# Performance work log

Hardware: AMD Instinct MI355X
Metric: run time of the kernel (lower is better)

Reference implementation:

```python
import jax, jax.numpy as jnp
import numpy as np

HEAD = 4

def setup_inputs() -> dict:
    key = jax.random.key(0)
    ks = jax.random.split(key, 6)
    b, h, w, dim, attn_dim = 2, 64, 64, 256, 128
    return {
        "query": jax.random.normal(ks[0], (b, h, w, dim), jnp.float32),
        "context": jax.random.normal(ks[1], (b, h, w, dim), jnp.float32),
        "Wq": jax.random.normal(ks[2], (dim, attn_dim), jnp.float32) * (dim ** -0.5),
        "Wk": jax.random.normal(ks[3], (dim, attn_dim), jnp.float32) * (dim ** -0.5),
        "Wv": jax.random.normal(ks[4], (dim, attn_dim), jnp.float32) * (dim ** -0.5),
        "Wo": jax.random.normal(ks[5], (attn_dim, dim), jnp.float32) * (attn_dim ** -0.5),
    }

def reference(query, context, Wq, Wk, Wv, Wo):
    b, h, w, c = query.shape
    attn_dim = Wq.shape[1]
    head = HEAD
    head_dim = attn_dim // head
    scale = head_dim ** -0.5
    n = h * w
    # 1x1 conv, no bias == per-pixel dense projection
    q = (query.reshape(b, n, c) @ Wq).reshape(b, n, head, head_dim)
    k = (context.reshape(b, n, c) @ Wk).reshape(b, n, head, head_dim)
    v = (context.reshape(b, n, c) @ Wv).reshape(b, n, head, head_dim)
    score = jnp.einsum('bihd,bjhd->bijh', q, k) * scale  # [b, n, n, head]
    attn = jax.nn.softmax(score, axis=-2)  # softmax over key axis j
    out = jnp.einsum('bijh,bjhd->bihd', attn, v).reshape(b, n, attn_dim)
    return (out @ Wo).reshape(b, h, w, c)
```

## Files before the change

### kernel.cpp

```cpp
#include <hip/hip_runtime.h>
#include <hip/hip_bf16.h>
#include <math.h>

#define N_TOK 4096
#define C_DIM 256
#define A_DIM 128
#define HEADS 4
#define HD    32
#define NBAT  2
#define BH    (NBAT * HEADS)

#define SCALE_LOG2E 0.25503521f

#define SPLITS 8
#define KEYS_PER_SPLIT (N_TOK / SPLITS)

#define KS 40
#define VS 72
#define PS 40

typedef __attribute__((ext_vector_type(8))) short short8;
typedef __attribute__((ext_vector_type(4))) short short4_t;
typedef __attribute__((ext_vector_type(4))) float floatx4;

__device__ __forceinline__ unsigned short f2bf(float f) {
    unsigned int u = __float_as_uint(f);
    u = (u + 0x7fffu + ((u >> 16) & 1u)) >> 16;
    return (unsigned short)u;
}
__device__ __forceinline__ float bf2f(unsigned short u) {
    return __uint_as_float((unsigned int)u << 16);
}
__device__ __forceinline__ unsigned int pack2(float a, float b) {
    unsigned int lo = (__float_as_uint(a) + 0x8000u) >> 16;
    unsigned int hi = (__float_as_uint(b) + 0x8000u) & 0xffff0000u;
    return hi | lo;
}

__global__ __launch_bounds__(256) void wpack_kernel(
    const float* __restrict__ Wq, const float* __restrict__ Wk,
    const float* __restrict__ Wv, const float* __restrict__ Wo,
    unsigned short* __restrict__ Wp)
{
    const int chunk = blockIdx.x * 256 + threadIdx.x;
    const int wid = chunk >> 12;
    const int c = chunk & 4095;
    const int lane = c & 63, quad = lane >> 4, l15 = lane & 15;
    short8 v;
    if (wid < 3) {
        const int s = c >> 9, t = (c >> 6) & 7;
        const float* W = (wid == 0) ? Wq : ((wid == 1) ? Wk : Wv);
        const float scale = (wid == 0) ? SCALE_LOG2E : 1.0f;
        const int src = (s * 32 + quad * 8) * A_DIM + t * 16 + l15;
        #pragma unroll
        for (int j = 0; j < 8; j++) v[j] = (short)f2bf(W[src + j * A_DIM] * scale);
    } else {
        const int s = c >> 10, t = (c >> 6) & 15;
        const int src = (s * 32 + quad * 8) * C_DIM + t * 16 + l15;
        #pragma unroll
        for (int j = 0; j < 8; j++) v[j] = (short)f2bf(Wo[src + j * C_DIM]);
    }
    *(short8*)(Wp + (long)chunk * 8) = v;
}

__global__ __launch_bounds__(256) void qkv_kernel(
    const float* __restrict__ query, const float* __restrict__ context,
    const unsigned short* __restrict__ Wp,
    unsigned short* __restrict__ Qb, unsigned short* __restrict__ Kb,
    unsigned short* __restrict__ Vb)
{
    __shared__ __align__(16) unsigned short V_lds[128 * 18];

    const int tid = threadIdx.x;
    const int w = tid >> 6, lane = tid & 63;
    const int quad = lane >> 4, l15 = lane & 15;
    const int ch = w;
    const long i0 = (long)blockIdx.x * 16;
    const long row = i0 + l15;

    const unsigned short* Wqp = Wp;
    const unsigned short* Wkp = Wp + 32768;
    const unsigned short* Wvp = Wp + 65536;

    floatx4 aQ[2] = {}, aK[2] = {}, aV[2] = {};

    for (int s = 0; s < 8; s++) {
        const float* qp = query + row * C_DIM + s * 32 + quad * 8;
        const float* cp = context + row * C_DIM + s * 32 + quad * 8;
        floatx4 q0 = *(const floatx4*)qp, q1 = *(const floatx4*)(qp + 4);
        floatx4 c0 = *(const floatx4*)cp, c1 = *(const floatx4*)(cp + 4);
        short8 aq, ac;
        #pragma unroll
        for (int j = 0; j < 4; j++) {
            aq[j] = (short)f2bf(q0[j]); aq[4 + j] = (short)f2bf(q1[j]);
            ac[j] = (short)f2bf(c0[j]); ac[4 + j] = (short)f2bf(c1[j]);
        }
        #pragma unroll
        for (int tp = 0; tp < 2; tp++) {
            const long fo = ((long)(s * 8 + ch * 2 + tp) * 64 + lane) * 8;
            short8 bq = *(const short8*)(Wqp + fo);
            short8 bk = *(const short8*)(Wkp + fo);
            short8 bv = *(const short8*)(Wvp + fo);
            aQ[tp] = __builtin_amdgcn_mfma_f32_16x16x32_bf16(aq, bq, aQ[tp], 0, 0, 0);
            aK[tp] = __builtin_amdgcn_mfma_f32_16x16x32_bf16(ac, bk, aK[tp], 0, 0, 0);
            aV[tp] = __builtin_amdgcn_mfma_f32_16x16x32_bf16(ac, bv, aV[tp], 0, 0, 0);
        }
    }

    const long b = i0 >> 12;
    const long n0 = i0 & (N_TOK - 1);
    const long nbase = n0 + quad * 4;
    #pragma unroll
    for (int tp = 0; tp < 2; tp++) {
        const int col = ch * 32 + tp * 16 + l15;
        const int h = col >> 5, d = col & 31;
        unsigned short* qdst = Qb + ((b * HEADS + h) * N_TOK + nbase) * HD + d;
        unsigned short* kdst = Kb + ((b * HEADS + h) * N_TOK + nbase) * HD + d;
        #pragma unroll
        for (int r = 0; r < 4; r++) {
            qdst[r * HD] = f2bf(aQ[tp][r]);
            kdst[r * HD] = f2bf(aK[tp][r]);
        }
        short4_t pv;
        #pragma unroll
        for (int r = 0; r < 4; r++) pv[r] = (short)f2bf(aV[tp][r]);
        *(short4_t*)&V_lds[col * 18 + quad * 4] = pv;
    }
    __syncthreads();

    {
        const int col = tid >> 1, seg = tid & 1;
        const int h = col >> 5, d = col & 31;
        unsigned short* dst = Vb + ((b * HEADS + h) * HD + d) * N_TOK + n0 + seg * 8;
        *(short8*)dst = *(const short8*)&V_lds[col * 18 + seg * 8];
    }
}

__global__ __launch_bounds__(256, 4) void attn_kernel(
    const unsigned short* __restrict__ Qb, const unsigned short* __restrict__ Kb,
    const unsigned short* __restrict__ Vb,
    unsigned short* __restrict__ AO, float* __restrict__ Lbuf)
{
    __shared__ __align__(16) unsigned short K_lds[64 * KS];
    __shared__ __align__(16) unsigned short V_lds[HD * VS];
    __shared__ __align__(16) unsigned short P_lds[4][2][2 * 16 * PS];

    const int tid  = threadIdx.x;
    const int w    = tid >> 6;
    const int lane = tid & 63;
    const int quad = lane >> 4;
    const int l15  = lane & 15;

    const int L  = blockIdx.x;
    const int g  = (L & 7) + 8 * ((L >> 3) >> 5);
    const int qb = (L >> 3) & 31;
    const int bh = g & 7;
    const int z  = g >> 3;
    const int i0 = qb * 128 + w * 32;

    const unsigned short* Qh = Qb + (long)bh * N_TOK * HD;
    const unsigned short* Kh = Kb + (long)bh * N_TOK * HD;
    const unsigned short* Vh = Vb + (long)bh * HD * N_TOK;

    const short8 qfA = *(const short8*)(Qh + (long)(i0 + l15) * HD + quad * 8);
    const short8 qfB = *(const short8*)(Qh + (long)(i0 + 16 + l15) * HD + quad * 8);

    floatx4 accA0 = {0.f,0.f,0.f,0.f}, accA1 = {0.f,0.f,0.f,0.f};
    floatx4 accB0 = {0.f,0.f,0.f,0.f}, accB1 = {0.f,0.f,0.f,0.f};
    float lAc = 0.f, lBc = 0.f;

    const int  kst = (tid >> 2) * KS + (tid & 3) * 8;
    const int  vst = (tid >> 3) * VS + (tid & 7) * 8;
    const long vgl = (long)(tid >> 3) * N_TOK + (tid & 7) * 8;
    const int  pwb = l15 * (PS / 2);

    const int j_lo = z * KEYS_PER_SPLIT, j_hi = j_lo + KEYS_PER_SPLIT;

    short8 kreg = *(const short8*)(Kh + (long)j_lo * HD + tid * 8);
    short8 vreg = *(const short8*)(Vh + vgl + j_lo);

    for (int j0 = j_lo; j0 < j_hi; j0 += 64) {
        __syncthreads();
        *(short8*)&K_lds[kst] = kreg;
        *(short8*)&V_lds[vst] = vreg;
        if (j0 + 64 < j_hi) {
            kreg = *(const short8*)(Kh + (long)(j0 + 64) * HD + tid * 8);
            vreg = *(const short8*)(Vh + vgl + j0 + 64);
        }
        __syncthreads();

        #pragma unroll
        for (int sub = 0; sub < 2; sub++) {
            const int jb = sub * 32;
            short8 kf0 = *(short8*)&K_lds[(jb + l15) * KS + quad * 8];
            short8 kf1 = *(short8*)&K_lds[(jb + 16 + l15) * KS + quad * 8];
            const floatx4 zf = {0.f,0.f,0.f,0.f};
            floatx4 sA0 = __builtin_amdgcn_mfma_f32_16x16x32_bf16(kf0, qfA, zf, 0, 0, 0);
            floatx4 sA1 = __builtin_amdgcn_mfma_f32_16x16x32_bf16(kf1, qfA, zf, 0, 0, 0);
            floatx4 sB0 = __builtin_amdgcn_mfma_f32_16x16x32_bf16(kf0, qfB, zf, 0, 0, 0);
            floatx4 sB1 = __builtin_amdgcn_mfma_f32_16x16x32_bf16(kf1, qfB, zf, 0, 0, 0);

            floatx4 pA0, pA1, pB0, pB1;
            #pragma unroll
            for (int r = 0; r < 4; r++) {
                pA0[r] = __builtin_amdgcn_exp2f(sA0[r]);
                pA1[r] = __builtin_amdgcn_exp2f(sA1[r]);
                pB0[r] = __builtin_amdgcn_exp2f(sB0[r]);
                pB1[r] = __builtin_amdgcn_exp2f(sB1[r]);
                lAc += pA0[r] + pA1[r];
                lBc += pB0[r] + pB1[r];
            }

            unsigned int* Pq = (unsigned int*)&P_lds[w][sub][0];
            Pq[pwb + quad * 2 + 0]       = pack2(pA0[0], pA0[1]);
            Pq[pwb + quad * 2 + 1]       = pack2(pA0[2], pA0[3]);
            Pq[pwb + 8 + quad * 2 + 0]   = pack2(pA1[0], pA1[1]);
            Pq[pwb + 8 + quad * 2 + 1]   = pack2(pA1[2], pA1[3]);
            Pq[320 + pwb + quad * 2 + 0] = pack2(pB0[0], pB0[1]);
            Pq[320 + pwb + quad * 2 + 1] = pack2(pB0[2], pB0[3]);
            Pq[320 + pwb + 8 + quad * 2 + 0] = pack2(pB1[0], pB1[1]);
            Pq[320 + pwb + 8 + quad * 2 + 1] = pack2(pB1[2], pB1[3]);

            short8 pfA = *(short8*)&P_lds[w][sub][l15 * PS + quad * 8];
            short8 pfB = *(short8*)&P_lds[w][sub][16 * PS + l15 * PS + quad * 8];

            short8 vf0 = *(short8*)&V_lds[l15 * VS + jb + quad * 8];
            short8 vf1 = *(short8*)&V_lds[(16 + l15) * VS + jb + quad * 8];
            accA0 = __builtin_amdgcn_mfma_f32_16x16x32_bf16(pfA, vf0, accA0, 0, 0, 0);
            accA1 = __builtin_amdgcn_mfma_f32_16x16x32_bf16(pfA, vf1, accA1, 0, 0, 0);
            accB0 = __builtin_amdgcn_mfma_f32_16x16x32_bf16(pfB, vf0, accB0, 0, 0, 0);
            accB1 = __builtin_amdgcn_mfma_f32_16x16x32_bf16(pfB, vf1, accB1, 0, 0, 0);
        }
    }

    lAc += __shfl_xor(lAc, 16); lAc += __shfl_xor(lAc, 32);
    lBc += __shfl_xor(lBc, 16); lBc += __shfl_xor(lBc, 32);

    const int b = bh >> 2, h = bh & 3;
    unsigned short* AOz = AO + (long)z * (NBAT * N_TOK * A_DIM);
    float* Lz = Lbuf + (long)z * (BH * N_TOK);
    if (quad == 0) {
        Lz[(long)bh * N_TOK + i0 + l15]      = lAc;
        Lz[(long)bh * N_TOK + i0 + 16 + l15] = lBc;
    }
    #pragma unroll
    for (int r = 0; r < 4; r++) {
        const float invA = 1.0f / __shfl(lAc, quad * 4 + r);
        const float invB = 1.0f / __shfl(lBc, quad * 4 + r);
        const long rowA = (long)b * N_TOK + i0 + quad * 4 + r;
        const long rowB = rowA + 16;
        AOz[rowA * A_DIM + h * HD + l15]      = f2bf(accA0[r] * invA);
        AOz[rowA * A_DIM + h * HD + 16 + l15] = f2bf(accA1[r] * invA);
        AOz[rowB * A_DIM + h * HD + l15]      = f2bf(accB0[r] * invB);
        AOz[rowB * A_DIM + h * HD + 16 + l15] = f2bf(accB1[r] * invB);
    }
}

__global__ __launch_bounds__(256) void outproj_kernel(
    const unsigned short* __restrict__ AO, const float* __restrict__ Lbuf,
    const unsigned short* __restrict__ Wp, float* __restrict__ out)
{
    const int tid = threadIdx.x;
    const int w = tid >> 6, lane = tid & 63;
    const int quad = lane >> 4, l15 = lane & 15;
    const int ch = w;
    const long i0 = (long)blockIdx.x * 16;
    const long row = i0 + l15;
    const int b = (int)(row >> 12);
    const int n = (int)(row & (N_TOK - 1));
    const unsigned short* Wop = Wp + 98304;

    floatx4 acc[4] = {};

    #pragma unroll
    for (int s = 0; s < 4; s++) {
        float lz[SPLITS], lsum = 0.f;
        #pragma unroll
        for (int z = 0; z < SPLITS; z++) {
            lz[z] = Lbuf[(long)z * (BH * N_TOK) + (long)(b * HEADS + s) * N_TOK + n];
            lsum += lz[z];
        }
        const float inv = 1.0f / lsum;
        float vals[8] = {};
        #pragma unroll
        for (int z = 0; z < SPLITS; z++) {
            short8 az = *(const short8*)(AO + (long)z * (NBAT * N_TOK * A_DIM) +
                                         row * A_DIM + s * 32 + quad * 8);
            const float wz = lz[z] * inv;
            #pragma unroll
            for (int j = 0; j < 8; j++) vals[j] += wz * bf2f((unsigned short)az[j]);
        }
        short8 af;
        #pragma unroll
        for (int j = 0; j < 8; j++) af[j] = (short)f2bf(vals[j]);
        #pragma unroll
        for (int tp = 0; tp < 4; tp++) {
            const int t = ch * 4 + tp;
            short8 bo = *(const short8*)(Wop + ((long)(s * 16 + t) * 64 + lane) * 8);
            acc[tp] = __builtin_amdgcn_mfma_f32_16x16x32_bf16(af, bo, acc[tp], 0, 0, 0);
        }
    }

    #pragma unroll
    for (int tp = 0; tp < 4; tp++) {
        #pragma unroll
        for (int r = 0; r < 4; r++)
            out[(i0 + quad * 4 + r) * C_DIM + (ch * 4 + tp) * 16 + l15] = acc[tp][r];
    }
}

extern "C" void kernel_launch(void* const* d_in, const int* in_sizes, int n_in,
                              void* d_out, int out_size, void* d_ws, size_t ws_size,
                              hipStream_t stream)
{
    const float* query   = (const float*)d_in[0];
    const float* context = (const float*)d_in[1];
    const float* Wq      = (const float*)d_in[2];
    const float* Wk      = (const float*)d_in[3];
    const float* Wv      = (const float*)d_in[4];
    const float* Wo      = (const float*)d_in[5];
    float* out = (float*)d_out;

    char* ws = (char*)d_ws;
    unsigned short* Qb = (unsigned short*)(ws);
    unsigned short* Kb = (unsigned short*)(ws + (2 << 20));
    unsigned short* Vb = (unsigned short*)(ws + (4 << 20));
    unsigned short* AO = (unsigned short*)(ws + (6 << 20));
    float*          Lb = (float*)(ws + (22 << 20));
    unsigned short* Wp = (unsigned short*)(ws + (23 << 20));

    wpack_kernel<<<dim3(64), dim3(256), 0, stream>>>(Wq, Wk, Wv, Wo, Wp);
    qkv_kernel<<<dim3(512), dim3(256), 0, stream>>>(query, context, Wp, Qb, Kb, Vb);
    attn_kernel<<<dim3(32 * BH * SPLITS), dim3(256), 0, stream>>>(
        Qb, Kb, Vb, AO, Lb);
    outproj_kernel<<<dim3(512), dim3(256), 0, stream>>>(AO, Lb, Wp, out);
}
```

Baseline: 125.7 us.

## Double per-wave query rows in attention to reuse K/V tiles across more queries

```diff
diff --git a/kernel.cpp b/kernel.cpp
--- a/kernel.cpp
+++ b/kernel.cpp
@@ -22,6 +22,7 @@
 typedef __attribute__((ext_vector_type(8))) short short8;
 typedef __attribute__((ext_vector_type(4))) short short4_t;
 typedef __attribute__((ext_vector_type(4))) float floatx4;
+typedef __attribute__((ext_vector_type(2))) unsigned int uint2v;
 
 __device__ __forceinline__ unsigned short f2bf(float f) {
     unsigned int u = __float_as_uint(f);
@@ -136,14 +137,14 @@
     }
 }
 
-__global__ __launch_bounds__(256, 4) void attn_kernel(
+__global__ __launch_bounds__(256, 2) void attn_kernel(
     const unsigned short* __restrict__ Qb, const unsigned short* __restrict__ Kb,
     const unsigned short* __restrict__ Vb,
     unsigned short* __restrict__ AO, float* __restrict__ Lbuf)
 {
     __shared__ __align__(16) unsigned short K_lds[64 * KS];
     __shared__ __align__(16) unsigned short V_lds[HD * VS];
-    __shared__ __align__(16) unsigned short P_lds[4][2][2 * 16 * PS];
+    __shared__ __align__(16) unsigned short P_lds[4][64 * PS];
 
     const int tid  = threadIdx.x;
     const int w    = tid >> 6;
@@ -152,27 +153,28 @@
     const int l15  = lane & 15;
 
     const int L  = blockIdx.x;
-    const int g  = (L & 7) + 8 * ((L >> 3) >> 5);
-    const int qb = (L >> 3) & 31;
+    const int qb = (L >> 3) & 15;
+    const int g  = (L & 7) + 8 * (L >> 7);
     const int bh = g & 7;
     const int z  = g >> 3;
-    const int i0 = qb * 128 + w * 32;
+    const int i0 = qb * 256 + w * 64;
 
     const unsigned short* Qh = Qb + (long)bh * N_TOK * HD;
     const unsigned short* Kh = Kb + (long)bh * N_TOK * HD;
     const unsigned short* Vh = Vb + (long)bh * HD * N_TOK;
 
-    const short8 qfA = *(const short8*)(Qh + (long)(i0 + l15) * HD + quad * 8);
-    const short8 qfB = *(const short8*)(Qh + (long)(i0 + 16 + l15) * HD + quad * 8);
-
-    floatx4 accA0 = {0.f,0.f,0.f,0.f}, accA1 = {0.f,0.f,0.f,0.f};
-    floatx4 accB0 = {0.f,0.f,0.f,0.f}, accB1 = {0.f,0.f,0.f,0.f};
-    float lAc = 0.f, lBc = 0.f;
+    short8 qf[4];
+    #pragma unroll
+    for (int t = 0; t < 4; t++)
+        qf[t] = *(const short8*)(Qh + (long)(i0 + t * 16 + l15) * HD + quad * 8);
+
+    floatx4 acc[4][2] = {};
+    float lc[4] = {0.f, 0.f, 0.f, 0.f};
 
     const int  kst = (tid >> 2) * KS + (tid & 3) * 8;
     const int  vst = (tid >> 3) * VS + (tid & 7) * 8;
     const long vgl = (long)(tid >> 3) * N_TOK + (tid & 7) * 8;
-    const int  pwb = l15 * (PS / 2);
+    unsigned int* Pq = (unsigned int*)&P_lds[w][0];
 
     const int j_lo = z * KEYS_PER_SPLIT, j_hi = j_lo + KEYS_PER_SPLIT;
 
@@ -192,67 +194,71 @@
         #pragma unroll
         for (int sub = 0; sub < 2; sub++) {
             const int jb = sub * 32;
-            short8 kf0 = *(short8*)&K_lds[(jb + l15) * KS + quad * 8];
-            short8 kf1 = *(short8*)&K_lds[(jb + 16 + l15) * KS + quad * 8];
             const floatx4 zf = {0.f,0.f,0.f,0.f};
-            floatx4 sA0 = __builtin_amdgcn_mfma_f32_16x16x32_bf16(kf0, qfA, zf, 0, 0, 0);
-            floatx4 sA1 = __builtin_amdgcn_mfma_f32_16x16x32_bf16(kf1, qfA, zf, 0, 0, 0);
-            floatx4 sB0 = __builtin_amdgcn_mfma_f32_16x16x32_bf16(kf0, qfB, zf, 0, 0, 0);
-            floatx4 sB1 = __builtin_amdgcn_mfma_f32_16x16x32_bf16(kf1, qfB, zf, 0, 0, 0);
-
-            floatx4 pA0, pA1, pB0, pB1;
-            #pragma unroll
-            for (int r = 0; r < 4; r++) {
-                pA0[r] = __builtin_amdgcn_exp2f(sA0[r]);
-                pA1[r] = __builtin_amdgcn_exp2f(sA1[r]);
-                pB0[r] = __builtin_amdgcn_exp2f(sB0[r]);
-                pB1[r] = __builtin_amdgcn_exp2f(sB1[r]);
-                lAc += pA0[r] + pA1[r];
-                lBc += pB0[r] + pB1[r];
+
+            {
+                short8 kf = *(short8*)&K_lds[(jb + l15) * KS + quad * 8];
+                #pragma unroll
+                for (int t = 0; t < 4; t++) {
+                    floatx4 s = __builtin_amdgcn_mfma_f32_16x16x32_bf16(kf, qf[t], zf, 0, 0, 0);
+                    float p0 = __builtin_amdgcn_exp2f(s[0]);
+                    float p1 = __builtin_amdgcn_exp2f(s[1]);
+                    float p2 = __builtin_amdgcn_exp2f(s[2]);
+                    float p3 = __builtin_amdgcn_exp2f(s[3]);
+                    lc[t] += (p0 + p1) + (p2 + p3);
+                    uint2v pk; pk[0] = pack2(p0, p1); pk[1] = pack2(p2, p3);
+                    *(uint2v*)&Pq[(t * 16 + l15) * 20 + quad * 2] = pk;
+                }
             }
-
-            unsigned int* Pq = (unsigned int*)&P_lds[w][sub][0];
-            Pq[pwb + quad * 2 + 0]       = pack2(pA0[0], pA0[1]);
-            Pq[pwb + quad * 2 + 1]       = pack2(pA0[2], pA0[3]);
-            Pq[pwb + 8 + quad * 2 + 0]   = pack2(pA1[0], pA1[1]);
-            Pq[pwb + 8 + quad * 2 + 1]   = pack2(pA1[2], pA1[3]);
-            Pq[320 + pwb + quad * 2 + 0] = pack2(pB0[0], pB0[1]);
-            Pq[320 + pwb + quad * 2 + 1] = pack2(pB0[2], pB0[3]);
-            Pq[320 + pwb + 8 + quad * 2 + 0] = pack2(pB1[0], pB1[1]);
-            Pq[320 + pwb + 8 + quad * 2 + 1] = pack2(pB1[2], pB1[3]);
-
-            short8 pfA = *(short8*)&P_lds[w][sub][l15 * PS + quad * 8];
-            short8 pfB = *(short8*)&P_lds[w][sub][16 * PS + l15 * PS + quad * 8];
+            {
+                short8 kf = *(short8*)&K_lds[(jb + 16 + l15) * KS + quad * 8];
+                #pragma unroll
+                for (int t = 0; t < 4; t++) {
+                    floatx4 s = __builtin_amdgcn_mfma_f32_16x16x32_bf16(kf, qf[t], zf, 0, 0, 0);
+                    float p0 = __builtin_amdgcn_exp2f(s[0]);
+                    float p1 = __builtin_amdgcn_exp2f(s[1]);
+                    float p2 = __builtin_amdgcn_exp2f(s[2]);
+                    float p3 = __builtin_amdgcn_exp2f(s[3]);
+                    lc[t] += (p0 + p1) + (p2 + p3);
+                    uint2v pk; pk[0] = pack2(p0, p1); pk[1] = pack2(p2, p3);
+                    *(uint2v*)&Pq[(t * 16 + l15) * 20 + 8 + quad * 2] = pk;
+                }
+            }
 
             short8 vf0 = *(short8*)&V_lds[l15 * VS + jb + quad * 8];
             short8 vf1 = *(short8*)&V_lds[(16 + l15) * VS + jb + quad * 8];
-            accA0 = __builtin_amdgcn_mfma_f32_16x16x32_bf16(pfA, vf0, accA0, 0, 0, 0);
-            accA1 = __builtin_amdgcn_mfma_f32_16x16x32_bf16(pfA, vf1, accA1, 0, 0, 0);
-            accB0 = __builtin_amdgcn_mfma_f32_16x16x32_bf16(pfB, vf0, accB0, 0, 0, 0);
-            accB1 = __builtin_amdgcn_mfma_f32_16x16x32_bf16(pfB, vf1, accB1, 0, 0, 0);
-        }
-    }
-
-    lAc += __shfl_xor(lAc, 16); lAc += __shfl_xor(lAc, 32);
-    lBc += __shfl_xor(lBc, 16); lBc += __shfl_xor(lBc, 32);
+            #pragma unroll
+            for (int t = 0; t < 4; t++) {
+                short8 pf = *(short8*)&P_lds[w][(t * 16 + l15) * PS + quad * 8];
+                acc[t][0] = __builtin_amdgcn_mfma_f32_16x16x32_bf16(pf, vf0, acc[t][0], 0, 0, 0);
+                acc[t][1] = __builtin_amdgcn_mfma_f32_16x16x32_bf16(pf, vf1, acc[t][1], 0, 0, 0);
+            }
+        }
+    }
+
+    #pragma unroll
+    for (int t = 0; t < 4; t++) {
+        lc[t] += __shfl_xor(lc[t], 16);
+        lc[t] += __shfl_xor(lc[t], 32);
+    }
 
     const int b = bh >> 2, h = bh & 3;
     unsigned short* AOz = AO + (long)z * (NBAT * N_TOK * A_DIM);
     float* Lz = Lbuf + (long)z * (BH * N_TOK);
     if (quad == 0) {
-        Lz[(long)bh * N_TOK + i0 + l15]      = lAc;
-        Lz[(long)bh * N_TOK + i0 + 16 + l15] = lBc;
-    }
-    #pragma unroll
-    for (int r = 0; r < 4; r++) {
-        const float invA = 1.0f / __shfl(lAc, quad * 4 + r);
-        const float invB = 1.0f / __shfl(lBc, quad * 4 + r);
-        const long rowA = (long)b * N_TOK + i0 + quad * 4 + r;
-        const long rowB = rowA + 16;
-        AOz[rowA * A_DIM + h * HD + l15]      = f2bf(accA0[r] * invA);
-        AOz[rowA * A_DIM + h * HD + 16 + l15] = f2bf(accA1[r] * invA);
-        AOz[rowB * A_DIM + h * HD + l15]      = f2bf(accB0[r] * invB);
-        AOz[rowB * A_DIM + h * HD + 16 + l15] = f2bf(accB1[r] * invB);
+        #pragma unroll
+        for (int t = 0; t < 4; t++)
+            Lz[(long)bh * N_TOK + i0 + t * 16 + l15] = lc[t];
+    }
+    #pragma unroll
+    for (int t = 0; t < 4; t++) {
+        #pragma unroll
+        for (int r = 0; r < 4; r++) {
+            const float inv = 1.0f / __shfl(lc[t], quad * 4 + r);
+            const long row = (long)b * N_TOK + i0 + t * 16 + quad * 4 + r;
+            AOz[row * A_DIM + h * HD + l15]      = f2bf(acc[t][0][r] * inv);
+            AOz[row * A_DIM + h * HD + 16 + l15] = f2bf(acc[t][1][r] * inv);
+        }
     }
 }
 
@@ -331,7 +337,7 @@
 
     wpack_kernel<<<dim3(64), dim3(256), 0, stream>>>(Wq, Wk, Wv, Wo, Wp);
     qkv_kernel<<<dim3(512), dim3(256), 0, stream>>>(query, context, Wp, Qb, Kb, Vb);
-    attn_kernel<<<dim3(32 * BH * SPLITS), dim3(256), 0, stream>>>(
+    attn_kernel<<<dim3(16 * BH * SPLITS), dim3(256), 0, stream>>>(
         Qb, Kb, Vb, AO, Lb);
     outproj_kernel<<<dim3(512), dim3(256), 0, stream>>>(AO, Lb, Wp, out);
 }
```

Result: no change. 127.9 us (+1.8%).

## Split QKV and output projection kernels across column halves to double grid size

Applied to the files above, without the earlier changes.

```diff
diff --git a/kernel.cpp b/kernel.cpp
--- a/kernel.cpp
+++ b/kernel.cpp
@@ -22,11 +22,10 @@
 typedef __attribute__((ext_vector_type(8))) short short8;
 typedef __attribute__((ext_vector_type(4))) short short4_t;
 typedef __attribute__((ext_vector_type(4))) float floatx4;
+typedef __attribute__((ext_vector_type(2))) unsigned int uint2v;
 
 __device__ __forceinline__ unsigned short f2bf(float f) {
-    unsigned int u = __float_as_uint(f);
-    u = (u + 0x7fffu + ((u >> 16) & 1u)) >> 16;
-    return (unsigned short)u;
+    return (unsigned short)((__float_as_uint(f) + 0x8000u) >> 16);
 }
 __device__ __forceinline__ float bf2f(unsigned short u) {
     return __uint_as_float((unsigned int)u << 16);
@@ -69,20 +68,22 @@
     unsigned short* __restrict__ Qb, unsigned short* __restrict__ Kb,
     unsigned short* __restrict__ Vb)
 {
-    __shared__ __align__(16) unsigned short V_lds[128 * 18];
+    __shared__ __align__(16) unsigned short V_lds[64 * 18];
 
     const int tid = threadIdx.x;
     const int w = tid >> 6, lane = tid & 63;
     const int quad = lane >> 4, l15 = lane & 15;
-    const int ch = w;
-    const long i0 = (long)blockIdx.x * 16;
+    const int bx = blockIdx.x;
+    const int cg = bx & 1;
+    const int t_col = cg * 4 + w;
+    const long i0 = (long)(bx >> 1) * 16;
     const long row = i0 + l15;
 
     const unsigned short* Wqp = Wp;
     const unsigned short* Wkp = Wp + 32768;
     const unsigned short* Wvp = Wp + 65536;
 
-    floatx4 aQ[2] = {}, aK[2] = {}, aV[2] = {};
+    floatx4 aQ = {0.f,0.f,0.f,0.f}, aK = {0.f,0.f,0.f,0.f}, aV = {0.f,0.f,0.f,0.f};
 
     for (int s = 0; s < 8; s++) {
         const float* qp = query + row * C_DIM + s * 32 + quad * 8;
@@ -95,44 +96,41 @@
             aq[j] = (short)f2bf(q0[j]); aq[4 + j] = (short)f2bf(q1[j]);
             ac[j] = (short)f2bf(c0[j]); ac[4 + j] = (short)f2bf(c1[j]);
         }
-        #pragma unroll
-        for (int tp = 0; tp < 2; tp++) {
-            const long fo = ((long)(s * 8 + ch * 2 + tp) * 64 + lane) * 8;
-            short8 bq = *(const short8*)(Wqp + fo);
-            short8 bk = *(const short8*)(Wkp + fo);
-            short8 bv = *(const short8*)(Wvp + fo);
-            aQ[tp] = __builtin_amdgcn_mfma_f32_16x16x32_bf16(aq, bq, aQ[tp], 0, 0, 0);
-            aK[tp] = __builtin_amdgcn_mfma_f32_16x16x32_bf16(ac, bk, aK[tp], 0, 0, 0);
-            aV[tp] = __builtin_amdgcn_mfma_f32_16x16x32_bf16(ac, bv, aV[tp], 0, 0, 0);
-        }
+        const long fo = ((long)(s * 8 + t_col) * 64 + lane) * 8;
+        short8 bq = *(const short8*)(Wqp + fo);
+        short8 bk = *(const short8*)(Wkp + fo);
+        short8 bv = *(const short8*)(Wvp + fo);
+        aQ = __builtin_amdgcn_mfma_f32_16x16x32_bf16(aq, bq, aQ, 0, 0, 0);
+        aK = __builtin_amdgcn_mfma_f32_16x16x32_bf16(ac, bk, aK, 0, 0, 0);
+        aV = __builtin_amdgcn_mfma_f32_16x16x32_bf16(ac, bv, aV, 0, 0, 0);
     }
 
     const long b = i0 >> 12;
     const long n0 = i0 & (N_TOK - 1);
     const long nbase = n0 + quad * 4;
-    #pragma unroll
-    for (int tp = 0; tp < 2; tp++) {
-        const int col = ch * 32 + tp * 16 + l15;
+    {
+        const int col = t_col * 16 + l15;
         const int h = col >> 5, d = col & 31;
         unsigned short* qdst = Qb + ((b * HEADS + h) * N_TOK + nbase) * HD + d;
         unsigned short* kdst = Kb + ((b * HEADS + h) * N_TOK + nbase) * HD + d;
         #pragma unroll
         for (int r = 0; r < 4; r++) {
-            qdst[r * HD] = f2bf(aQ[tp][r]);
-            kdst[r * HD] = f2bf(aK[tp][r]);
+            qdst[r * HD] = f2bf(aQ[r]);
+            kdst[r * HD] = f2bf(aK[r]);
         }
         short4_t pv;
         #pragma unroll
-        for (int r = 0; r < 4; r++) pv[r] = (short)f2bf(aV[tp][r]);
-        *(short4_t*)&V_lds[col * 18 + quad * 4] = pv;
+        for (int r = 0; r < 4; r++) pv[r] = (short)f2bf(aV[r]);
+        *(short4_t*)&V_lds[(w * 16 + l15) * 18 + quad * 4] = pv;
     }
     __syncthreads();
 
     {
-        const int col = tid >> 1, seg = tid & 1;
+        const int lc = tid >> 2, seg = tid & 3;
+        const int col = cg * 64 + lc;
         const int h = col >> 5, d = col & 31;
-        unsigned short* dst = Vb + ((b * HEADS + h) * HD + d) * N_TOK + n0 + seg * 8;
-        *(short8*)dst = *(const short8*)&V_lds[col * 18 + seg * 8];
+        unsigned short* dst = Vb + ((b * HEADS + h) * HD + d) * N_TOK + n0 + seg * 4;
+        *(short4_t*)dst = *(const short4_t*)&V_lds[lc * 18 + seg * 4];
     }
 }
 
@@ -152,7 +150,7 @@
     const int l15  = lane & 15;
 
     const int L  = blockIdx.x;
-    const int g  = (L & 7) + 8 * ((L >> 3) >> 5);
+    const int g  = (L & 7) + 8 * (L >> 8);
     const int qb = (L >> 3) & 31;
     const int bh = g & 7;
     const int z  = g >> 3;
@@ -212,14 +210,14 @@
             }
 
             unsigned int* Pq = (unsigned int*)&P_lds[w][sub][0];
-            Pq[pwb + quad * 2 + 0]       = pack2(pA0[0], pA0[1]);
-            Pq[pwb + quad * 2 + 1]       = pack2(pA0[2], pA0[3]);
-            Pq[pwb + 8 + quad * 2 + 0]   = pack2(pA1[0], pA1[1]);
-            Pq[pwb + 8 + quad * 2 + 1]   = pack2(pA1[2], pA1[3]);
-            Pq[320 + pwb + quad * 2 + 0] = pack2(pB0[0], pB0[1]);
-            Pq[320 + pwb + quad * 2 + 1] = pack2(pB0[2], pB0[3]);
-            Pq[320 + pwb + 8 + quad * 2 + 0] = pack2(pB1[0], pB1[1]);
-            Pq[320 + pwb + 8 + quad * 2 + 1] = pack2(pB1[2], pB1[3]);
+            { uint2v pk; pk[0] = pack2(pA0[0], pA0[1]); pk[1] = pack2(pA0[2], pA0[3]);
+              *(uint2v*)&Pq[pwb + quad * 2] = pk; }
+            { uint2v pk; pk[0] = pack2(pA1[0], pA1[1]); pk[1] = pack2(pA1[2], pA1[3]);
+              *(uint2v*)&Pq[pwb + 8 + quad * 2] = pk; }
+            { uint2v pk; pk[0] = pack2(pB0[0], pB0[1]); pk[1] = pack2(pB0[2], pB0[3]);
+              *(uint2v*)&Pq[320 + pwb + quad * 2] = pk; }
+            { uint2v pk; pk[0] = pack2(pB1[0], pB1[1]); pk[1] = pack2(pB1[2], pB1[3]);
+              *(uint2v*)&Pq[320 + pwb + 8 + quad * 2] = pk; }
 
             short8 pfA = *(short8*)&P_lds[w][sub][l15 * PS + quad * 8];
             short8 pfB = *(short8*)&P_lds[w][sub][16 * PS + l15 * PS + quad * 8];
@@ -263,14 +261,15 @@
     const int tid = threadIdx.x;
     const int w = tid >> 6, lane = tid & 63;
     const int quad = lane >> 4, l15 = lane & 15;
-    const int ch = w;
-    const long i0 = (long)blockIdx.x * 16;
+    const int bx = blockIdx.x;
+    const int cg = bx & 1;
+    const long i0 = (long)(bx >> 1) * 16;
     const long row = i0 + l15;
     const int b = (int)(row >> 12);
     const int n = (int)(row & (N_TOK - 1));
     const unsigned short* Wop = Wp + 98304;
 
-    floatx4 acc[4] = {};
+    floatx4 acc[2] = {};
 
     #pragma unroll
     for (int s = 0; s < 4; s++) {
@@ -294,18 +293,19 @@
         #pragma unroll
         for (int j = 0; j < 8; j++) af[j] = (short)f2bf(vals[j]);
         #pragma unroll
-        for (int tp = 0; tp < 4; tp++) {
-            const int t = ch * 4 + tp;
+        for (int tp = 0; tp < 2; tp++) {
+            const int t = cg * 8 + w * 2 + tp;
             short8 bo = *(const short8*)(Wop + ((long)(s * 16 + t) * 64 + lane) * 8);
             acc[tp] = __builtin_amdgcn_mfma_f32_16x16x32_bf16(af, bo, acc[tp], 0, 0, 0);
         }
     }
 
     #pragma unroll
-    for (int tp = 0; tp < 4; tp++) {
+    for (int tp = 0; tp < 2; tp++) {
+        const int t = cg * 8 + w * 2 + tp;
         #pragma unroll
         for (int r = 0; r < 4; r++)
-            out[(i0 + quad * 4 + r) * C_DIM + (ch * 4 + tp) * 16 + l15] = acc[tp][r];
+            out[(i0 + quad * 4 + r) * C_DIM + t * 16 + l15] = acc[tp][r];
     }
 }
 
@@ -330,8 +330,8 @@
     unsigned short* Wp = (unsigned short*)(ws + (23 << 20));
 
     wpack_kernel<<<dim3(64), dim3(256), 0, stream>>>(Wq, Wk, Wv, Wo, Wp);
-    qkv_kernel<<<dim3(512), dim3(256), 0, stream>>>(query, context, Wp, Qb, Kb, Vb);
+    qkv_kernel<<<dim3(1024), dim3(256), 0, stream>>>(query, context, Wp, Qb, Kb, Vb);
     attn_kernel<<<dim3(32 * BH * SPLITS), dim3(256), 0, stream>>>(
         Qb, Kb, Vb, AO, Lb);
-    outproj_kernel<<<dim3(512), dim3(256), 0, stream>>>(AO, Lb, Wp, out);
-}
+    outproj_kernel<<<dim3(1024), dim3(256), 0, stream>>>(AO, Lb, Wp, out);
+}
```

After: 142.8 us. +13.6%, slower.
